# Kernel tuning notes

Hardware: AMD Instinct MI355X
Metric: run time of the kernel (lower is better)

The kernel has to match this reference:

```python
import jax, jax.numpy as jnp
import numpy as np

NUM_HEADS = 16
HIDDEN = 1024
EPS = 1e-5


def _layernorm(x, g, b):
    mu = jnp.mean(x, axis=-1, keepdims=True)
    var = jnp.mean((x - mu) ** 2, axis=-1, keepdims=True)
    return (x - mu) * jax.lax.rsqrt(var + EPS) * g + b


def setup_inputs() -> dict:
    key = jax.random.key(0)
    ks = jax.random.split(key, 10)
    B, S, H = 2, 2048, HIDDEN
    s = 0.02
    d = {
        "X": jax.random.normal(ks[0], (B, S, H), jnp.float32),
        "Wq": jax.random.normal(ks[1], (H, H), jnp.float32) * s,
        "bq": jnp.zeros((H,), jnp.float32),
        "Wk": jax.random.normal(ks[2], (H, H), jnp.float32) * s,
        "bk": jnp.zeros((H,), jnp.float32),
        "Wv": jax.random.normal(ks[3], (H, H), jnp.float32) * s,
        "bv": jnp.zeros((H,), jnp.float32),
        "Wo": jax.random.normal(ks[4], (H, H), jnp.float32) * s,
        "bo": jnp.zeros((H,), jnp.float32),
        "ln1_g": jnp.ones((H,), jnp.float32),
        "ln1_b": jnp.zeros((H,), jnp.float32),
        "Wup": jax.random.normal(ks[5], (4 * H, H), jnp.float32) * s,
        "bup": jnp.zeros((4 * H,), jnp.float32),
        "Wdown": jax.random.normal(ks[6], (H, 4 * H), jnp.float32) * s,
        "bdown": jnp.zeros((H,), jnp.float32),
        "ln2_g": jnp.ones((H,), jnp.float32),
        "ln2_b": jnp.zeros((H,), jnp.float32),
    }
    return d


def reference(X, Wq, bq, Wk, bk, Wv, bv, Wo, bo, ln1_g, ln1_b,
              Wup, bup, Wdown, bdown, ln2_g, ln2_b):
    B, S, H = X.shape
    nh = NUM_HEADS
    hd = H // nh
    # QKV projections -> [B, nh, S, hd]
    q = (X @ Wq.T + bq).reshape(B, S, nh, hd).transpose(0, 2, 1, 3)
    k = (X @ Wk.T + bk).reshape(B, S, nh, hd).transpose(0, 2, 1, 3)
    v = (X @ Wv.T + bv).reshape(B, S, nh, hd).transpose(0, 2, 1, 3)
    scores = jnp.einsum("bhqd,bhkd->bhqk", q, k) / jnp.sqrt(jnp.float32(hd))
    causal = jnp.tril(jnp.ones((S, S), dtype=bool))
    scores = jnp.where(causal, scores, jnp.float32(-1e20))
    att = jax.nn.softmax(scores, axis=-1)  # dropout p=0 (eval)
    mid = jnp.einsum("bhqk,bhkd->bhqd", att, v)  # [B, nh, S, hd]
    mid = mid.transpose(0, 2, 1, 3).reshape(B, S, H)
    att_out = mid @ Wo.T + bo
    h = _layernorm(X + att_out, ln1_g, ln1_b)
    up = jax.nn.relu(h @ Wup.T + bup)
    down = up @ Wdown.T + bdown
    return _layernorm(h + down, ln2_g, ln2_b)
```

## Files before the change

kernel.cpp:

```cpp
#include <hip/hip_runtime.h>

#define B_ 2
#define S_ 2048
#define H_ 1024
#define NH 16
#define HD 64
#define LN_EPS 1e-5f

typedef unsigned short u16;
typedef unsigned int u32;
typedef __attribute__((ext_vector_type(8))) short bf16x8;
typedef __attribute__((ext_vector_type(4))) float f32x4;
typedef __attribute__((ext_vector_type(16))) float f32x16;
typedef __attribute__((ext_vector_type(4))) u32 u32x4;
typedef __attribute__((ext_vector_type(4))) u16 u16x4;

__device__ __forceinline__ u16 f2bf(float f) {
  u32 u = __float_as_uint(f);
  u32 r = (u + 0x7FFFu + ((u >> 16) & 1u)) >> 16;
  return (u16)r;
}
__device__ __forceinline__ float bflo(u32 w) { return __uint_as_float(w << 16); }
__device__ __forceinline__ float bfhi(u32 w) { return __uint_as_float(w & 0xffff0000u); }

__device__ __forceinline__ void gload_lds16(const void* g, void* l) {
  __builtin_amdgcn_global_load_lds(
      (const __attribute__((address_space(1))) void*)(uintptr_t)g,
      (__attribute__((address_space(3))) void*)(uintptr_t)l, 16, 0, 0);
}

__global__ __launch_bounds__(256) void k_cvt(const float* __restrict__ in,
                                             u16* __restrict__ out, int n4) {
  int i = blockIdx.x * 256 + threadIdx.x;
  if (i >= n4) return;
  f32x4 v = ((const f32x4*)in)[i];
  u16x4 o = { f2bf(v[0]), f2bf(v[1]), f2bf(v[2]), f2bf(v[3]) };
  ((u16x4*)out)[i] = o;
}

__global__ __launch_bounds__(256) void k_pack3(const float* __restrict__ a,
                                               const float* __restrict__ b,
                                               const float* __restrict__ c,
                                               float* __restrict__ o) {
  int i = blockIdx.x * 256 + threadIdx.x;
  if (i >= 3 * H_) return;
  o[i] = (i < H_) ? a[i] : (i < 2 * H_ ? b[i - H_] : c[i - 2 * H_]);
}

template<int RELU, int F32OUT, int BF16OUT, int BIAS>
__global__ __launch_bounds__(512, 2) void k_gemm8(const u16* __restrict__ A,
                                                  const u16* __restrict__ W,
                                                  const float* __restrict__ bias,
                                                  float* __restrict__ outf,
                                                  u16* __restrict__ outb,
                                                  int M, int N, int lda, int ldb,
                                                  int Kc, int tilesM) {
  extern __shared__ u16 lds[];
  const int tid = threadIdx.x, lane = tid & 63, wid = tid >> 6;
  const int wr = wid >> 2, wc = wid & 3;
  const int lr = lane & 15, lk = lane >> 4;

  const int nwg = gridDim.x;
  const int bid = blockIdx.x;
  const int lid = (bid & 7) * (nwg >> 3) + (bid >> 3);
  const int ty = lid % tilesM;
  const int txz = lid / tilesM;
  const int tilesN = N >> 8;
  const int tx = txz % tilesN;
  const int kz = txz / tilesN;
  const int row0 = ty << 8, col0 = tx << 8;
  A += (size_t)kz * Kc;
  W += (size_t)kz * Kc;
  const size_t outoff = (size_t)kz * M * N;

  const int NT = Kc >> 6;

  f32x4 acc[8][4];
#pragma unroll
  for (int i = 0; i < 8; ++i)
#pragma unroll
    for (int j = 0; j < 4; ++j) acc[i][j] = (f32x4){0.f, 0.f, 0.f, 0.f};

  const int srow = tid >> 3;
  const int csw8 = ((tid & 7) ^ (srow & 7)) << 3;

  auto stage_ht = [&](int ht) {
    const int t = ht >> 2, sel = ht & 3;
    const int mat = (sel < 2) ? 1 : 0;
    const int hh = sel & 1;
    const u16* g = mat ? W : A;
    const int ld = mat ? ldb : lda;
    const int b0 = mat ? col0 : row0;
    const int kt = t << 6;
    u16* dst = lds + ((t & 1) << 15) + (mat << 14) + (hh << 13) + tid * 8;
#pragma unroll
    for (int j = 0; j < 2; ++j) {
      const int r = (hh << 7) + (j << 6) + srow;
      gload_lds16(g + (size_t)(b0 + r) * ld + kt + csw8, dst + (j << 12));
    }
  };

  union UU { u32x4 u; bf16x8 b; };
  auto ldvec = [&](const u16* base, int r, int c) -> bf16x8 {
    UU x;
    x.u = *(const u32x4*)(base + r * 64 + ((c ^ (r & 7)) << 3));
    return x.b;
  };

#pragma unroll
  for (int i = 0; i < 4; ++i) stage_ht(i);
  asm volatile("s_waitcnt vmcnt(0)" ::: "memory");
  __builtin_amdgcn_s_barrier();

  for (int t = 0; t < NT; ++t) {
    const u16* SA = lds + ((t & 1) << 15);
    const u16* SB = SA + 16384;
#pragma unroll
    for (int ph = 0; ph < 4; ++ph) {
      const int mh = ph >> 1, ks = ph & 1;
      const int c = (ks << 2) + lk;
      bf16x8 bb[4], aa[4];
#pragma unroll
      for (int ni = 0; ni < 4; ++ni)
        bb[ni] = ldvec(SB, (wc << 6) + (ni << 4) + lr, c);
#pragma unroll
      for (int mi = 0; mi < 4; ++mi)
        aa[mi] = ldvec(SA, (wr << 7) + (mh << 6) + (mi << 4) + lr, c);
      if (t + 1 < NT && ph < 2) {
        stage_ht(4 * (t + 1) + 2 * ph);
        stage_ht(4 * (t + 1) + 2 * ph + 1);
      }
      __builtin_amdgcn_s_barrier();
      __builtin_amdgcn_s_setprio(1);
#pragma unroll
      for (int mi = 0; mi < 4; ++mi)
#pragma unroll
        for (int ni = 0; ni < 4; ++ni)
          acc[(mh << 2) + mi][ni] = __builtin_amdgcn_mfma_f32_16x16x32_bf16(
              aa[mi], bb[ni], acc[(mh << 2) + mi][ni], 0, 0, 0);
      __builtin_amdgcn_s_setprio(0);
      if (ph == 3)
        asm volatile("s_waitcnt vmcnt(0)" ::: "memory");
      __builtin_amdgcn_s_barrier();
    }
  }

  float bs[4] = {0.f, 0.f, 0.f, 0.f};
  if (BIAS) {
#pragma unroll
    for (int ni = 0; ni < 4; ++ni)
      bs[ni] = bias[col0 + (wc << 6) + (ni << 4) + lr];
  }
#pragma unroll
  for (int mi = 0; mi < 8; ++mi) {
#pragma unroll
    for (int ni = 0; ni < 4; ++ni) {
#pragma unroll
      for (int r = 0; r < 4; ++r) {
        int row = row0 + (wr << 7) + (mi << 4) + (lk << 2) + r;
        int col = col0 + (wc << 6) + (ni << 4) + lr;
        float v = acc[mi][ni][r] + bs[ni];
        if (RELU) v = fmaxf(v, 0.f);
        if (F32OUT) outf[outoff + (size_t)row * N + col] = v;
        if (BF16OUT) outb[outoff + (size_t)row * N + col] = f2bf(v);
      }
    }
  }
}

__global__ __launch_bounds__(256) void k_vt(const u16* __restrict__ QKV,
                                            u16* __restrict__ vt) {
  __shared__ u16 T[64 * 64];
  const int tid = threadIdx.x;
  const int s0 = blockIdx.x * 64;
  const int bh = blockIdx.y;
  const int b = bh >> 4, h = bh & 15;
#pragma unroll
  for (int p = 0; p < 2; ++p) {
    int id = p * 256 + tid;
    int r = id >> 3, c = id & 7;
    u32x4 v = *(const u32x4*)(QKV + (size_t)(b * S_ + s0 + r) * 3072 + 2048 + h * 64 + c * 8);
    int sw = (r ^ (r >> 3)) & 7;
    *(u32x4*)(T + r * 64 + ((c ^ sw) << 3)) = v;
  }
  __syncthreads();
#pragma unroll
  for (int p = 0; p < 2; ++p) {
    int id = p * 256 + tid;
    int d = id >> 3, cs = id & 7;
    u16 tmp[8];
#pragma unroll
    for (int k = 0; k < 8; ++k) {
      int r = cs * 8 + k;
      int sw = (r ^ (r >> 3)) & 7;
      tmp[k] = T[r * 64 + ((((d >> 3) ^ sw)) << 3) + (d & 7)];
    }
    *(u32x4*)(vt + ((size_t)bh * 64 + d) * 2048 + s0 + cs * 8) = *(const u32x4*)tmp;
  }
}

__global__ __launch_bounds__(256) void k_attn_mfma(const u16* __restrict__ QKV,
                                                   const u16* __restrict__ Vt,
                                                   u16* __restrict__ mid) {
  __shared__ u16 lds[16384];
  const int tid = threadIdx.x, lane = tid & 63, wid = tid >> 6;
  const int lq = lane & 31, lh = lane >> 5;
  const int qb = (S_ / 128 - 1) - blockIdx.x;
  const int bh = blockIdx.y;
  const int b = bh >> 4, h = bh & 15;
  const int q0w = qb * 128 + wid * 32;
  const int qg = q0w + lq;

  const int srow = tid >> 3, sc = tid & 7;
  const int ssw = ((sc ^ (srow & 7)) << 3);
  const u16* srcK = QKV + (size_t)b * S_ * 3072 + 1024 + h * 64;
  const u16* srcV = Vt + (size_t)bh * 64 * 2048;

  auto stage = [&](int kv, int slot) {
    u16* dK = lds + slot * 8192 + tid * 8;
    u16* dV = dK + 4096;
    const u16* sk = srcK + (size_t)(kv * 64 + srow) * 3072 + ssw;
    const u16* sv = srcV + (size_t)srow * 2048 + kv * 64 + ssw;
    gload_lds16(sk, dK);
    gload_lds16(sk + (size_t)32 * 3072, dK + 2048);
    gload_lds16(sv, dV);
    gload_lds16(sv + (size_t)32 * 2048, dV + 2048);
  };

  union U { u32x4 u; bf16x8 b; };
  U qf[4];
#pragma unroll
  for (int ks = 0; ks < 4; ++ks) {
    const size_t off = (size_t)(b * S_ + qg) * 3072 + h * HD + ks * 16 + lh * 8;
    u32x4 u = *(const u32x4*)(QKV + off);
    u32x4 s;
#pragma unroll
    for (int t = 0; t < 4; ++t) {
      u32 lo = (u32)f2bf(bflo(u[t]) * 0.125f);
      u32 hi = (u32)f2bf(bfhi(u[t]) * 0.125f);
      s[t] = lo | (hi << 16);
    }
    qf[ks].u = s;
  }

  float m = -1e30f, l = 0.f;
  f32x16 acc[2];
#pragma unroll
  for (int mo = 0; mo < 2; ++mo)
#pragma unroll
    for (int r = 0; r < 16; ++r) acc[mo][r] = 0.f;

  const int nt = qb * 2 + 2;

  stage(0, 0);
  asm volatile("s_waitcnt vmcnt(0)" ::: "memory");
  __builtin_amdgcn_s_barrier();

  for (int kv = 0; kv < nt; ++kv) {
    const int kv0 = kv * 64;
    const int cur = kv & 1;
    if (kv + 1 < nt) stage(kv + 1, cur ^ 1);

    if (kv0 <= q0w + 31) {
      const u16* Ks = lds + cur * 8192;
      const u16* Vs = Ks + 4096;

      f32x16 sf[2];
#pragma unroll
      for (int nf = 0; nf < 2; ++nf)
#pragma unroll
        for (int r = 0; r < 16; ++r) sf[nf][r] = 0.f;
#pragma unroll
      for (int ks = 0; ks < 4; ++ks) {
#pragma unroll
        for (int nf = 0; nf < 2; ++nf) {
          int r = nf * 32 + lq;
          int c = ks * 2 + lh;
          U kf;
          kf.u = *(const u32x4*)(Ks + r * 64 + ((c ^ (r & 7)) << 3));
          sf[nf] = __builtin_amdgcn_mfma_f32_32x32x16_bf16(kf.b, qf[ks].b, sf[nf], 0, 0, 0);
        }
      }

      if (kv0 + 63 > q0w) {
#pragma unroll
        for (int nf = 0; nf < 2; ++nf)
#pragma unroll
          for (int r = 0; r < 16; ++r) {
            int kvg = kv0 + nf * 32 + (r & 3) + 8 * (r >> 2) + 4 * lh;
            if (kvg > qg) sf[nf][r] = -1e30f;
          }
      }

      float tm = sf[0][0];
#pragma unroll
      for (int r = 1; r < 16; ++r) tm = fmaxf(tm, sf[0][r]);
#pragma unroll
      for (int r = 0; r < 16; ++r) tm = fmaxf(tm, sf[1][r]);
      tm = fmaxf(tm, __shfl_xor(tm, 32));
      const float mn = fmaxf(m, tm);
      const float corr = __expf(m - mn);
      m = mn;
      float rs = 0.f;
#pragma unroll
      for (int nf = 0; nf < 2; ++nf)
#pragma unroll
        for (int r = 0; r < 16; ++r) {
          float p = __expf(sf[nf][r] - mn);
          sf[nf][r] = p;
          rs += p;
        }
      rs += __shfl_xor(rs, 32);
      l = l * corr + rs;
#pragma unroll
      for (int mo = 0; mo < 2; ++mo)
#pragma unroll
        for (int r = 0; r < 16; ++r) acc[mo][r] *= corr;

      u32 q32[2][8];
#pragma unroll
      for (int nf = 0; nf < 2; ++nf)
#pragma unroll
        for (int i = 0; i < 8; ++i)
          asm("v_cvt_pk_bf16_f32 %0, %1, %2"
              : "=v"(q32[nf][i]) : "v"(sf[nf][2 * i]), "v"(sf[nf][2 * i + 1]));

#pragma unroll
      for (int s = 0; s < 4; ++s) {
        const int nfp = s >> 1, sg = s & 1;
        u32 x = q32[nfp][4 * sg + 0];
        u32 y = q32[nfp][4 * sg + 1];
        u32 z = q32[nfp][4 * sg + 2];
        u32 w = q32[nfp][4 * sg + 3];
        asm("v_permlane32_swap_b32 %0, %1" : "+v"(x), "+v"(z));
        asm("v_permlane32_swap_b32 %0, %1" : "+v"(y), "+v"(w));
        U pb;
        pb.u = (u32x4){x, y, z, w};
#pragma unroll
        for (int mo = 0; mo < 2; ++mo) {
          int r = mo * 32 + lq;
          int c = s * 2 + lh;
          U vv;
          vv.u = *(const u32x4*)(Vs + r * 64 + ((c ^ (r & 7)) << 3));
          acc[mo] = __builtin_amdgcn_mfma_f32_32x32x16_bf16(vv.b, pb.b, acc[mo], 0, 0, 0);
        }
      }
    }

    asm volatile("s_waitcnt vmcnt(0)" ::: "memory");
    __builtin_amdgcn_s_barrier();
  }

  u16* Ow = lds + wid * (32 * 72);
  const float inv = 1.f / l;
#pragma unroll
  for (int mo = 0; mo < 2; ++mo)
#pragma unroll
    for (int r = 0; r < 16; ++r) {
      int d = mo * 32 + (r & 3) + 8 * (r >> 2) + 4 * lh;
      Ow[lq * 72 + d] = f2bf(acc[mo][r] * inv);
    }
  __asm__ volatile("" ::: "memory");
#pragma unroll
  for (int r4 = 0; r4 < 4; ++r4) {
    int ql = r4 * 8 + (lane >> 3);
    int c = lane & 7;
    u32x4 v = *(const u32x4*)(Ow + ql * 72 + c * 8);
    *(u32x4*)(mid + (size_t)(b * S_ + q0w + ql) * H_ + h * HD + c * 8) = v;
  }
}

template<int BF16OUT, int NZ>
__global__ __launch_bounds__(256) void k_lnr(const float* __restrict__ a,
                                             const u16* __restrict__ P,
                                             const float* __restrict__ bd,
                                             const float* __restrict__ g,
                                             const float* __restrict__ bb,
                                             float* __restrict__ outf,
                                             u16* __restrict__ outb) {
  __shared__ float red[8];
  const int row = blockIdx.x, tid = threadIdx.x;
  const size_t base = (size_t)row * H_ + tid * 4;
  f32x4 t = *(const f32x4*)(a + base);
  f32x4 vb = *(const f32x4*)(bd + tid * 4);
  t += vb;
#pragma unroll
  for (int z = 0; z < NZ; ++z) {
    u16x4 p = *(const u16x4*)(P + (size_t)z * ((size_t)B_ * S_ * H_) + base);
#pragma unroll
    for (int e = 0; e < 4; ++e) t[e] += __uint_as_float((u32)p[e] << 16);
  }
  float sum = t[0] + t[1] + t[2] + t[3];
#pragma unroll
  for (int msk = 32; msk >= 1; msk >>= 1) sum += __shfl_xor(sum, msk, 64);
  if ((tid & 63) == 0) red[tid >> 6] = sum;
  __syncthreads();
  float mu = (red[0] + red[1] + red[2] + red[3]) * (1.f / H_);
  f32x4 d = t - mu;
  float sq = d[0] * d[0] + d[1] * d[1] + d[2] * d[2] + d[3] * d[3];
#pragma unroll
  for (int msk = 32; msk >= 1; msk >>= 1) sq += __shfl_xor(sq, msk, 64);
  if ((tid & 63) == 0) red[4 + (tid >> 6)] = sq;
  __syncthreads();
  float var = (red[4] + red[5] + red[6] + red[7]) * (1.f / H_);
  float rs = rsqrtf(var + LN_EPS);
  f32x4 gg = *(const f32x4*)(g + tid * 4);
  f32x4 bv = *(const f32x4*)(bb + tid * 4);
  f32x4 o = d * rs * gg + bv;
  *(f32x4*)(outf + base) = o;
  if (BF16OUT) {
    u16x4 ob = { f2bf(o[0]), f2bf(o[1]), f2bf(o[2]), f2bf(o[3]) };
    *(u16x4*)(outb + base) = ob;
  }
}

extern "C" void kernel_launch(void* const* d_in, const int* in_sizes, int n_in,
                              void* d_out, int out_size, void* d_ws, size_t ws_size,
                              hipStream_t stream) {
  const float* X   = (const float*)d_in[0];
  const float* Wq  = (const float*)d_in[1];
  const float* bq  = (const float*)d_in[2];
  const float* Wk  = (const float*)d_in[3];
  const float* bk  = (const float*)d_in[4];
  const float* Wv  = (const float*)d_in[5];
  const float* bv  = (const float*)d_in[6];
  const float* Wo  = (const float*)d_in[7];
  const float* bo  = (const float*)d_in[8];
  const float* g1  = (const float*)d_in[9];
  const float* b1  = (const float*)d_in[10];
  const float* Wup = (const float*)d_in[11];
  const float* bup = (const float*)d_in[12];
  const float* Wdn = (const float*)d_in[13];
  const float* bdn = (const float*)d_in[14];
  const float* g2  = (const float*)d_in[15];
  const float* b2  = (const float*)d_in[16];
  float* out = (float*)d_out;

  const size_t MS = (size_t)B_ * S_;
  const size_t nX = MS * H_;

  char* ws = (char*)d_ws;
  size_t off = 0;
  auto alloc = [&](size_t bytes) {
    char* p = ws + off;
    off += (bytes + 255) & ~(size_t)255;
    return p;
  };
  u16* Xb    = (u16*)alloc(nX * 2);
  u16* Wqkv  = (u16*)alloc((size_t)3 * H_ * H_ * 2);
  u16* Wob   = (u16*)alloc((size_t)H_ * H_ * 2);
  u16* Wupb  = (u16*)alloc((size_t)4 * H_ * H_ * 2);
  u16* Wdnb  = (u16*)alloc((size_t)4 * H_ * H_ * 2);
  float* bqkv = (float*)alloc(3 * H_ * 4);
  u16* QKVb  = (u16*)alloc(nX * 3 * 2);
  u16* midb  = (u16*)alloc(nX * 2);
  u16* Pbuf  = (u16*)alloc(nX * 4 * 2);
  float* h   = (float*)Xb;
  u16* upb   = QKVb;
  u16* vtb   = Pbuf;
  u16* WoP   = Pbuf;
  u16* hb    = Pbuf + nX * 2;
  u16* P     = Pbuf;

  dim3 blk(256);

  k_cvt<<<dim3(4096), blk, 0, stream>>>(X, Xb, (int)(nX / 4));
  k_cvt<<<dim3(1024), blk, 0, stream>>>(Wq, Wqkv, H_ * H_ / 4);
  k_cvt<<<dim3(1024), blk, 0, stream>>>(Wk, Wqkv + (size_t)H_ * H_, H_ * H_ / 4);
  k_cvt<<<dim3(1024), blk, 0, stream>>>(Wv, Wqkv + (size_t)2 * H_ * H_, H_ * H_ / 4);
  k_cvt<<<dim3(1024), blk, 0, stream>>>(Wo, Wob, H_ * H_ / 4);
  k_cvt<<<dim3(4096), blk, 0, stream>>>(Wup, Wupb, 4 * H_ * H_ / 4);
  k_cvt<<<dim3(4096), blk, 0, stream>>>(Wdn, Wdnb, 4 * H_ * H_ / 4);
  k_pack3<<<dim3(12), blk, 0, stream>>>(bq, bk, bv, bqkv);

  k_gemm8<0, 0, 1, 1><<<dim3(16 * 12), dim3(512), 131072, stream>>>(
      Xb, Wqkv, bqkv, nullptr, QKVb, (int)MS, 3 * H_, H_, H_, H_, 16);

  k_vt<<<dim3(S_ / 64, B_ * NH), blk, 0, stream>>>(QKVb, vtb);

  k_attn_mfma<<<dim3(S_ / 128, B_ * NH), blk, 0, stream>>>(QKVb, vtb, midb);

  k_gemm8<0, 0, 1, 0><<<dim3(16 * 4 * 2), dim3(512), 131072, stream>>>(
      midb, Wob, nullptr, nullptr, WoP, (int)MS, H_, H_, H_, 512, 16);

  k_lnr<1, 2><<<dim3(MS), blk, 0, stream>>>(X, WoP, bo, g1, b1, h, hb);

  k_gemm8<1, 0, 1, 1><<<dim3(16 * 16), dim3(512), 131072, stream>>>(
      hb, Wupb, bup, nullptr, upb, (int)MS, 4 * H_, H_, H_, H_, 16);

  k_gemm8<0, 0, 1, 0><<<dim3(16 * 4 * 4), dim3(512), 131072, stream>>>(
      upb, Wdnb, nullptr, nullptr, P, (int)MS, H_, 4 * H_, 4 * H_, H_, 16);

  k_lnr<0, 4><<<dim3(MS), blk, 0, stream>>>(h, P, bdn, g2, b2, out, nullptr);
}
```

Measured before the change: 251.1 us.

## Merge fp32-to-bf16 conversions into one launch and restructure attention loop

Replaces seven conversion launches with a single kernel that picks its source tensor by index range and writes one contiguous bf16 buffer. This relies on the destination buffers being laid out back to back. The attention kernel drops the double-buffered async global-to-LDS staging in favour of synchronous single-buffer loads, which shrinks LDS so three blocks can share a CU. It also adds s_setprio around the MFMA sections and a lazy softmax rescale that only corrects the accumulators when the row max grows by more than 8. The exchange is more occupancy and less rescale arithmetic, at the cost of losing load/compute overlap within each block and adding two barriers per KV tile.

```diff
diff --git a/kernel.cpp b/kernel.cpp
--- a/kernel.cpp
+++ b/kernel.cpp
@@ -29,13 +29,27 @@
       (__attribute__((address_space(3))) void*)(uintptr_t)l, 16, 0, 0);
 }
 
-__global__ __launch_bounds__(256) void k_cvt(const float* __restrict__ in,
-                                             u16* __restrict__ out, int n4) {
-  int i = blockIdx.x * 256 + threadIdx.x;
-  if (i >= n4) return;
-  f32x4 v = ((const f32x4*)in)[i];
+__global__ __launch_bounds__(256) void k_cvt_all(const float* __restrict__ X,
+                                                 const float* __restrict__ Wq,
+                                                 const float* __restrict__ Wk,
+                                                 const float* __restrict__ Wv,
+                                                 const float* __restrict__ Wo,
+                                                 const float* __restrict__ Wup,
+                                                 const float* __restrict__ Wdn,
+                                                 u16* __restrict__ dst) {
+  const int i = blockIdx.x * 256 + threadIdx.x;
+  const float* s;
+  int off;
+  if (i < 1048576)      { s = X;   off = 0; }
+  else if (i < 1310720) { s = Wq;  off = 1048576; }
+  else if (i < 1572864) { s = Wk;  off = 1310720; }
+  else if (i < 1835008) { s = Wv;  off = 1572864; }
+  else if (i < 2097152) { s = Wo;  off = 1835008; }
+  else if (i < 3145728) { s = Wup; off = 2097152; }
+  else                  { s = Wdn; off = 3145728; }
+  f32x4 v = ((const f32x4*)s)[i - off];
   u16x4 o = { f2bf(v[0]), f2bf(v[1]), f2bf(v[2]), f2bf(v[3]) };
-  ((u16x4*)out)[i] = o;
+  ((u16x4*)dst)[i] = o;
 }
 
 __global__ __launch_bounds__(256) void k_pack3(const float* __restrict__ a,
@@ -199,10 +213,12 @@
   }
 }
 
-__global__ __launch_bounds__(256) void k_attn_mfma(const u16* __restrict__ QKV,
-                                                   const u16* __restrict__ Vt,
-                                                   u16* __restrict__ mid) {
-  __shared__ u16 lds[16384];
+__global__ __launch_bounds__(256, 3) void k_attn_mfma(const u16* __restrict__ QKV,
+                                                      const u16* __restrict__ Vt,
+                                                      u16* __restrict__ mid) {
+  __shared__ u16 lds[9216];
+  u16* Ks = lds;
+  u16* Vs = lds + 4096;
   const int tid = threadIdx.x, lane = tid & 63, wid = tid >> 6;
   const int lq = lane & 31, lh = lane >> 5;
   const int qb = (S_ / 128 - 1) - blockIdx.x;
@@ -211,22 +227,6 @@
   const int q0w = qb * 128 + wid * 32;
   const int qg = q0w + lq;
 
-  const int srow = tid >> 3, sc = tid & 7;
-  const int ssw = ((sc ^ (srow & 7)) << 3);
-  const u16* srcK = QKV + (size_t)b * S_ * 3072 + 1024 + h * 64;
-  const u16* srcV = Vt + (size_t)bh * 64 * 2048;
-
-  auto stage = [&](int kv, int slot) {
-    u16* dK = lds + slot * 8192 + tid * 8;
-    u16* dV = dK + 4096;
-    const u16* sk = srcK + (size_t)(kv * 64 + srow) * 3072 + ssw;
-    const u16* sv = srcV + (size_t)srow * 2048 + kv * 64 + ssw;
-    gload_lds16(sk, dK);
-    gload_lds16(sk + (size_t)32 * 3072, dK + 2048);
-    gload_lds16(sv, dV);
-    gload_lds16(sv + (size_t)32 * 2048, dV + 2048);
-  };
-
   union U { u32x4 u; bf16x8 b; };
   U qf[4];
 #pragma unroll
@@ -251,106 +251,112 @@
     for (int r = 0; r < 16; ++r) acc[mo][r] = 0.f;
 
   const int nt = qb * 2 + 2;
-
-  stage(0, 0);
-  asm volatile("s_waitcnt vmcnt(0)" ::: "memory");
-  __builtin_amdgcn_s_barrier();
-
   for (int kv = 0; kv < nt; ++kv) {
     const int kv0 = kv * 64;
-    const int cur = kv & 1;
-    if (kv + 1 < nt) stage(kv + 1, cur ^ 1);
-
-    if (kv0 <= q0w + 31) {
-      const u16* Ks = lds + cur * 8192;
-      const u16* Vs = Ks + 4096;
-
-      f32x16 sf[2];
+    __syncthreads();
+#pragma unroll
+    for (int p = 0; p < 2; ++p) {
+      int id = p * 256 + tid;
+      int r = id >> 3, c = id & 7;
+      u32x4 ku = *(const u32x4*)(QKV + (size_t)(b * S_ + kv0 + r) * 3072 + 1024 + h * 64 + c * 8);
+      *(u32x4*)(Ks + r * 64 + ((c ^ (r & 7)) << 3)) = ku;
+      u32x4 vu = *(const u32x4*)(Vt + ((size_t)bh * 64 + r) * 2048 + kv0 + c * 8);
+      *(u32x4*)(Vs + r * 64 + ((c ^ (r & 7)) << 3)) = vu;
+    }
+    __syncthreads();
+
+    if (kv0 > q0w + 31) continue;
+
+    f32x16 sf[2];
+#pragma unroll
+    for (int nf = 0; nf < 2; ++nf)
+#pragma unroll
+      for (int r = 0; r < 16; ++r) sf[nf][r] = 0.f;
+    __builtin_amdgcn_s_setprio(1);
+#pragma unroll
+    for (int ks = 0; ks < 4; ++ks) {
+#pragma unroll
+      for (int nf = 0; nf < 2; ++nf) {
+        int r = nf * 32 + lq;
+        int c = ks * 2 + lh;
+        U kf;
+        kf.u = *(const u32x4*)(Ks + r * 64 + ((c ^ (r & 7)) << 3));
+        sf[nf] = __builtin_amdgcn_mfma_f32_32x32x16_bf16(kf.b, qf[ks].b, sf[nf], 0, 0, 0);
+      }
+    }
+    __builtin_amdgcn_s_setprio(0);
+
+    if (kv0 + 63 > q0w) {
 #pragma unroll
       for (int nf = 0; nf < 2; ++nf)
 #pragma unroll
-        for (int r = 0; r < 16; ++r) sf[nf][r] = 0.f;
-#pragma unroll
-      for (int ks = 0; ks < 4; ++ks) {
-#pragma unroll
-        for (int nf = 0; nf < 2; ++nf) {
-          int r = nf * 32 + lq;
-          int c = ks * 2 + lh;
-          U kf;
-          kf.u = *(const u32x4*)(Ks + r * 64 + ((c ^ (r & 7)) << 3));
-          sf[nf] = __builtin_amdgcn_mfma_f32_32x32x16_bf16(kf.b, qf[ks].b, sf[nf], 0, 0, 0);
+        for (int r = 0; r < 16; ++r) {
+          int kvg = kv0 + nf * 32 + (r & 3) + 8 * (r >> 2) + 4 * lh;
+          if (kvg > qg) sf[nf][r] = -1e30f;
         }
-      }
-
-      if (kv0 + 63 > q0w) {
-#pragma unroll
-        for (int nf = 0; nf < 2; ++nf)
-#pragma unroll
-          for (int r = 0; r < 16; ++r) {
-            int kvg = kv0 + nf * 32 + (r & 3) + 8 * (r >> 2) + 4 * lh;
-            if (kvg > qg) sf[nf][r] = -1e30f;
-          }
-      }
-
-      float tm = sf[0][0];
-#pragma unroll
-      for (int r = 1; r < 16; ++r) tm = fmaxf(tm, sf[0][r]);
-#pragma unroll
-      for (int r = 0; r < 16; ++r) tm = fmaxf(tm, sf[1][r]);
-      tm = fmaxf(tm, __shfl_xor(tm, 32));
+    }
+
+    float tm = sf[0][0];
+#pragma unroll
+    for (int r = 1; r < 16; ++r) tm = fmaxf(tm, sf[0][r]);
+#pragma unroll
+    for (int r = 0; r < 16; ++r) tm = fmaxf(tm, sf[1][r]);
+    tm = fmaxf(tm, __shfl_xor(tm, 32));
+    if (__any(tm - m > 8.f)) {
       const float mn = fmaxf(m, tm);
       const float corr = __expf(m - mn);
       m = mn;
-      float rs = 0.f;
-#pragma unroll
-      for (int nf = 0; nf < 2; ++nf)
-#pragma unroll
-        for (int r = 0; r < 16; ++r) {
-          float p = __expf(sf[nf][r] - mn);
-          sf[nf][r] = p;
-          rs += p;
-        }
-      rs += __shfl_xor(rs, 32);
-      l = l * corr + rs;
+      l *= corr;
 #pragma unroll
       for (int mo = 0; mo < 2; ++mo)
 #pragma unroll
         for (int r = 0; r < 16; ++r) acc[mo][r] *= corr;
-
-      u32 q32[2][8];
-#pragma unroll
-      for (int nf = 0; nf < 2; ++nf)
-#pragma unroll
-        for (int i = 0; i < 8; ++i)
-          asm("v_cvt_pk_bf16_f32 %0, %1, %2"
-              : "=v"(q32[nf][i]) : "v"(sf[nf][2 * i]), "v"(sf[nf][2 * i + 1]));
-
-#pragma unroll
-      for (int s = 0; s < 4; ++s) {
-        const int nfp = s >> 1, sg = s & 1;
-        u32 x = q32[nfp][4 * sg + 0];
-        u32 y = q32[nfp][4 * sg + 1];
-        u32 z = q32[nfp][4 * sg + 2];
-        u32 w = q32[nfp][4 * sg + 3];
-        asm("v_permlane32_swap_b32 %0, %1" : "+v"(x), "+v"(z));
-        asm("v_permlane32_swap_b32 %0, %1" : "+v"(y), "+v"(w));
-        U pb;
-        pb.u = (u32x4){x, y, z, w};
-#pragma unroll
-        for (int mo = 0; mo < 2; ++mo) {
-          int r = mo * 32 + lq;
-          int c = s * 2 + lh;
-          U vv;
-          vv.u = *(const u32x4*)(Vs + r * 64 + ((c ^ (r & 7)) << 3));
-          acc[mo] = __builtin_amdgcn_mfma_f32_32x32x16_bf16(vv.b, pb.b, acc[mo], 0, 0, 0);
-        }
+    }
+    float rs = 0.f;
+#pragma unroll
+    for (int nf = 0; nf < 2; ++nf)
+#pragma unroll
+      for (int r = 0; r < 16; ++r) {
+        float p = __expf(sf[nf][r] - m);
+        sf[nf][r] = p;
+        rs += p;
       }
-    }
-
-    asm volatile("s_waitcnt vmcnt(0)" ::: "memory");
-    __builtin_amdgcn_s_barrier();
-  }
-
+    rs += __shfl_xor(rs, 32);
+    l += rs;
+
+    u32 q32[2][8];
+#pragma unroll
+    for (int nf = 0; nf < 2; ++nf)
+#pragma unroll
+      for (int i = 0; i < 8; ++i)
+        asm("v_cvt_pk_bf16_f32 %0, %1, %2"
+            : "=v"(q32[nf][i]) : "v"(sf[nf][2 * i]), "v"(sf[nf][2 * i + 1]));
+
+    __builtin_amdgcn_s_setprio(1);
+#pragma unroll
+    for (int s = 0; s < 4; ++s) {
+      const int nfp = s >> 1, sg = s & 1;
+      u32 x = q32[nfp][4 * sg + 0];
+      u32 y = q32[nfp][4 * sg + 1];
+      u32 z = q32[nfp][4 * sg + 2];
+      u32 w = q32[nfp][4 * sg + 3];
+      asm("v_permlane32_swap_b32 %0, %1" : "+v"(x), "+v"(z));
+      asm("v_permlane32_swap_b32 %0, %1" : "+v"(y), "+v"(w));
+      U pb;
+      pb.u = (u32x4){x, y, z, w};
+#pragma unroll
+      for (int mo = 0; mo < 2; ++mo) {
+        int r = mo * 32 + lq;
+        int c = s * 2 + lh;
+        U vv;
+        vv.u = *(const u32x4*)(Vs + r * 64 + ((c ^ (r & 7)) << 3));
+        acc[mo] = __builtin_amdgcn_mfma_f32_32x32x16_bf16(vv.b, pb.b, acc[mo], 0, 0, 0);
+      }
+    }
+    __builtin_amdgcn_s_setprio(0);
+  }
+
+  __syncthreads();
   u16* Ow = lds + wid * (32 * 72);
   const float inv = 1.f / l;
 #pragma unroll
@@ -464,13 +470,7 @@
 
   dim3 blk(256);
 
-  k_cvt<<<dim3(4096), blk, 0, stream>>>(X, Xb, (int)(nX / 4));
-  k_cvt<<<dim3(1024), blk, 0, stream>>>(Wq, Wqkv, H_ * H_ / 4);
-  k_cvt<<<dim3(1024), blk, 0, stream>>>(Wk, Wqkv + (size_t)H_ * H_, H_ * H_ / 4);
-  k_cvt<<<dim3(1024), blk, 0, stream>>>(Wv, Wqkv + (size_t)2 * H_ * H_, H_ * H_ / 4);
-  k_cvt<<<dim3(1024), blk, 0, stream>>>(Wo, Wob, H_ * H_ / 4);
-  k_cvt<<<dim3(4096), blk, 0, stream>>>(Wup, Wupb, 4 * H_ * H_ / 4);
-  k_cvt<<<dim3(4096), blk, 0, stream>>>(Wdn, Wdnb, 4 * H_ * H_ / 4);
+  k_cvt_all<<<dim3(16384), blk, 0, stream>>>(X, Wq, Wk, Wv, Wo, Wup, Wdn, Xb);
   k_pack3<<<dim3(12), blk, 0, stream>>>(bq, bk, bv, bqkv);
 
   k_gemm8<0, 0, 1, 1><<<dim3(16 * 12), dim3(512), 131072, stream>>>(
```

New measurement: 231.4 us, median of 2. 7.8% less time.
